# Performance work log

Hardware: AMD Instinct MI355X
Metric: run time of the kernel (lower is better)

Reference implementation:

```python
import jax, jax.numpy as jnp
import numpy as np
import math

T, B, C, H, W = 1, 64, 512, 8, 8
E, NH, MEM, FF = 512, 8, 32, 2048
HD = E // NH            # 64 per-head channels
TOT = HD * H * W        # 4096 = flattened per-head dim (channels x spatial)


def conv2d(x, w, b):
    # NCHW conv with 'same' padding, matching torch.nn.Conv2d(padding='same')
    y = jax.lax.conv_general_dilated(x, w, (1, 1), 'SAME',
                                     dimension_numbers=('NCHW', 'OIHW', 'NCHW'))
    return y + b[None, :, None, None]


def layernorm(x, w, b, eps=1e-5):
    # LayerNorm over (C,H,W) with elementwise affine, matching nn.LayerNorm((C,H,W))
    m = jnp.mean(x, axis=(1, 2, 3), keepdims=True)
    v = jnp.var(x, axis=(1, 2, 3), keepdims=True)
    return (x - m) * jax.lax.rsqrt(v + eps) * w[None] + b[None]


def setup_inputs() -> dict:
    key = jax.random.key(0)
    ks = jax.random.split(key, 16)
    s = 0.02
    inp = {
        'input': jax.random.normal(ks[0], (T, B, C, H, W), jnp.float32),
        'attn_mask': jax.random.randint(ks[1], (B * NH, T, MEM), 0, 2) == 1,
        'concat_k': jax.random.normal(ks[2], (B, MEM, NH, TOT), jnp.float32),
        'concat_v': jax.random.normal(ks[3], (B, MEM, NH, TOT), jnp.float32),
        'proj_w': jax.random.normal(ks[4], (3 * E, C, 3, 3), jnp.float32) * s,
        'proj_b': jnp.zeros((3 * E,), jnp.float32),
        'out_w': jax.random.normal(ks[5], (E, E, 3, 3), jnp.float32) * s,
        'out_b': jnp.zeros((E,), jnp.float32),
        'lin1_w': jax.random.normal(ks[6], (FF, E, 3, 3), jnp.float32) * s,
        'lin1_b': jnp.zeros((FF,), jnp.float32),
        'lin2_w': jax.random.normal(ks[7], (E, FF, 3, 3), jnp.float32) * s,
        'lin2_b': jnp.zeros((E,), jnp.float32),
        'n1_w': jnp.ones((E, H, W), jnp.float32),
        'n1_b': jnp.zeros((E, H, W), jnp.float32),
        'n2_w': jnp.ones((E, H, W), jnp.float32),
        'n2_b': jnp.zeros((E, H, W), jnp.float32),
        'pos_w': jax.random.normal(ks[8], (MEM, H * W * E), jnp.float32) * s,
        'pos_b': jax.random.uniform(ks[9], (MEM, NH), jnp.float32, -0.1, 0.1),
    }
    return inp


def reference(input, attn_mask, concat_k, concat_v, proj_w, proj_b, out_w, out_b,
              lin1_w, lin1_b, lin2_w, lin2_b, n1_w, n1_b, n2_w, n2_b, pos_w, pos_b):
    x = input.reshape(T * B, C, H, W)
    kqv = conv2d(x, proj_w, proj_b)                      # [B, 3E, H, W]
    k0, q0, v0 = kqv[:, :E], kqv[:, E:2 * E], kqv[:, 2 * E:]

    def split_heads(t):  # [T*B,E,H,W] -> [B*NH, T, TOT]
        return t.reshape(T, B * NH, HD, H, W).transpose(1, 0, 2, 3, 4).reshape(B * NH, T, TOT)

    k, q, v = split_heads(k0), split_heads(q0), split_heads(v0)
    q = q / math.sqrt(TOT)

    def mem_pre(c):  # [B,MEM,NH,TOT] -> [B*NH, MEM-1, TOT]
        return c[:, 1:].transpose(1, 0, 2, 3).reshape(MEM - 1, B * NH, TOT).transpose(1, 0, 2)

    k = jnp.concatenate([mem_pre(concat_k), k], axis=1)  # [B*NH, MEM, TOT]
    v = jnp.concatenate([mem_pre(concat_v), v], axis=1)

    # learned relative-position bias on keys and logits
    pw = jnp.broadcast_to(pos_w[:, None, :], (MEM, B, NH * TOT)).reshape(MEM, B * NH, TOT).transpose(1, 0, 2)
    pb = jnp.broadcast_to(pos_b[:, None, :], (MEM, B, NH)).reshape(MEM, B * NH).transpose(1, 0)
    k = k + pw

    mask = jnp.where(attn_mask, -jnp.inf, 0.0).astype(q.dtype)
    mask = mask.at[:, :, -1].set(5.0)                    # current step always attendable (+5 bias)
    logits = mask + jnp.einsum('bqd,bkd->bqk', q, k) + pb[:, None, :]
    w_attn = jax.nn.softmax(logits, axis=-1)             # [B*NH, T, MEM]
    attn = jnp.einsum('bqk,bkd->bqd', w_attn, v)         # [B*NH, T, TOT]
    attn = attn.transpose(1, 0, 2).reshape(B, E, H, W)

    out = conv2d(attn, out_w, out_b)
    ret_k = k.transpose(1, 0, 2).reshape(MEM, B, NH, TOT).transpose(1, 0, 2, 3)
    ret_v = v.transpose(1, 0, 2).reshape(MEM, B, NH, TOT).transpose(1, 0, 2, 3)

    # norm_first=False path
    out = out + x[:, :E]
    out = layernorm(out, n1_w, n1_b)
    ff = conv2d(jax.nn.relu(conv2d(out, lin1_w, lin1_b)), lin2_w, lin2_b)
    out = layernorm(out + ff, n2_w, n2_b)
    return (out[None], ret_k, ret_v)
```

## Files before the change

### kernel.cpp

```cpp
#include <hip/hip_runtime.h>
#include <hip/hip_bf16.h>
#include <stdint.h>

typedef __attribute__((ext_vector_type(8))) short bf16x8;
typedef __attribute__((ext_vector_type(4))) float f32x4;

static __device__ __forceinline__ unsigned short f2bf(float f) {
  union { float f; unsigned int u; } v; v.f = f;
  unsigned int u = v.u;
  return (unsigned short)((u + 0x7FFFu + ((u >> 16) & 1u)) >> 16);
}

static __device__ __forceinline__ void gld16(const void* g, void* l) {
  __builtin_amdgcn_global_load_lds(
      (const __attribute__((address_space(1))) unsigned int*)g,
      (__attribute__((address_space(3))) unsigned int*)l, 16, 0, 0);
}

__global__ __launch_bounds__(256) void k_zero(uint4* __restrict__ p, int n) {
  int i = blockIdx.x * 256 + threadIdx.x;
  if (i < n) p[i] = make_uint4(0u, 0u, 0u, 0u);
}

__global__ __launch_bounds__(256) void k_prep(
    const float* __restrict__ projw, const float* __restrict__ outw,
    const float* __restrict__ l1w, const float* __restrict__ l2w,
    const float* __restrict__ x,
    unsigned short* __restrict__ wbP, unsigned short* __restrict__ wbO,
    unsigned short* __restrict__ wbL1, unsigned short* __restrict__ wbL2,
    unsigned short* __restrict__ xp) {
  __shared__ float l[4608];
  int bid = blockIdx.x, t = threadIdx.x;
  if (bid < 6144) {
    const float* in; unsigned short* out; int o, C, c0;
    if (bid < 1536)      { in = projw; out = wbP;  o = bid;               C = 512;  c0 = 0; }
    else if (bid < 2048) { in = outw;  out = wbO;  o = bid - 1536;        C = 512;  c0 = 0; }
    else if (bid < 4096) { in = l1w;   out = wbL1; o = bid - 2048;        C = 512;  c0 = 0; }
    else                 { in = l2w;   out = wbL2; o = (bid - 4096) >> 2; C = 2048; c0 = ((bid - 4096) & 3) << 9; }
    const float* src = in + ((size_t)o * C + c0) * 9;
    for (int j = t; j < 4608; j += 256) l[j] = src[j];
    __syncthreads();
    unsigned short* dst = out + (size_t)o * 9 * C;
#pragma unroll
    for (int j = 0; j < 18; ++j) {
      int f = t * 18 + j;
      int tap = f >> 9, c = f & 511;
      dst[(size_t)tap * C + c0 + c] = f2bf(l[c * 9 + tap]);
    }
  } else {
    int idx = bid - 6144;
    int b = idx >> 3, c0 = (idx & 7) << 6;
    float (*lt)[65] = (float(*)[65])l;
    int cr = t >> 2, p0 = (t & 3) << 4;
    const float* src = x + ((size_t)b * 512 + c0 + cr) * 64 + p0;
#pragma unroll
    for (int j = 0; j < 4; ++j) {
      float4 v = *(const float4*)(src + j * 4);
      lt[cr][p0 + j * 4 + 0] = v.x; lt[cr][p0 + j * 4 + 1] = v.y;
      lt[cr][p0 + j * 4 + 2] = v.z; lt[cr][p0 + j * 4 + 3] = v.w;
    }
    __syncthreads();
    int pix = t >> 2, cc0 = (t & 3) << 4;
    size_t prow = (size_t)b * 100 + 11 + (pix >> 3) * 10 + (pix & 7);
    unsigned short pk[16];
#pragma unroll
    for (int j = 0; j < 16; ++j) pk[j] = f2bf(lt[cc0 + j][pix]);
    *(uint4*)(xp + prow * 512 + c0 + cc0) = *(const uint4*)pk;
    *(uint4*)(xp + prow * 512 + c0 + cc0 + 8) = *(const uint4*)(pk + 8);
  }
}

__global__ __launch_bounds__(256) void k_x2pad(const float* __restrict__ x,
                                               unsigned short* __restrict__ xp) {
  int b = blockIdx.x >> 3, c0 = (blockIdx.x & 7) << 6;
  int t = threadIdx.x;
  __shared__ float l[64][65];
  int cr = t >> 2, p0 = (t & 3) << 4;
  const float* src = x + ((size_t)b * 512 + c0 + cr) * 64 + p0;
#pragma unroll
  for (int j = 0; j < 4; ++j) {
    float4 v = *(const float4*)(src + j * 4);
    l[cr][p0 + j * 4 + 0] = v.x; l[cr][p0 + j * 4 + 1] = v.y;
    l[cr][p0 + j * 4 + 2] = v.z; l[cr][p0 + j * 4 + 3] = v.w;
  }
  __syncthreads();
  int pix = t >> 2, cc0 = (t & 3) << 4;
  size_t prow = (size_t)b * 100 + 11 + (pix >> 3) * 10 + (pix & 7);
  unsigned short pk[16];
#pragma unroll
  for (int j = 0; j < 16; ++j) pk[j] = f2bf(l[cc0 + j][pix]);
  *(uint4*)(xp + prow * 512 + c0 + cc0) = *(const uint4*)pk;
  *(uint4*)(xp + prow * 512 + c0 + cc0 + 8) = *(const uint4*)(pk + 8);
}

template <int EPI>
__global__ __launch_bounds__(256, 2) void k_gemm9(
    const unsigned short* __restrict__ Wt, int ldK,
    const unsigned short* __restrict__ Xp, int C, int tlog,
    int kiter, const float* __restrict__ bias,
    void* __restrict__ outv, int Cout, size_t zstride) {
  __shared__ unsigned short lds[2][2][8192];
  int t = threadIdx.x, lane = t & 63, wid = t >> 6;

  int gx = gridDim.x;
  int f = blockIdx.x + blockIdx.y * gx;
  int cpx = (gx * gridDim.y) >> 3;
  int fs = (f & 7) * cpx + (f >> 3);
  int bx = fs % gx, by = fs / gx;

  int O0 = bx << 7, M0 = by << 7;
  int kbase = blockIdx.z * kiter;
  int srow = lane >> 3, skg = (lane & 7) << 3;

  int wrow[4], pbv[4];
#pragma unroll
  for (int i = 0; i < 4; ++i) {
    int rl = wid * 8 + i * 32 + srow;
    wrow[i] = O0 + rl;
    int m = M0 + rl, b = m >> 6, pix = m & 63;
    pbv[i] = b * 100 + (pix >> 3) * 10 + (pix & 7);
  }

  f32x4 acc[4][4];
#pragma unroll
  for (int i = 0; i < 4; ++i)
#pragma unroll
    for (int j = 0; j < 4; ++j) acc[i][j] = (f32x4){0.f, 0.f, 0.f, 0.f};

  auto stage = [&](int buf, int kt) {
    int gk = kbase + kt;
    int tap = gk >> tlog;
    int c0 = (gk - (tap << tlog)) << 6;
    int toff = tap + 7 * ((tap * 11) >> 5);
#pragma unroll
    for (int i = 0; i < 4; ++i) {
      gld16(Wt + (size_t)wrow[i] * ldK + (gk << 6) + skg,
            &lds[buf][0][(wid * 8 + i * 32) * 64]);
      gld16(Xp + (size_t)(pbv[i] + toff) * C + c0 + skg,
            &lds[buf][1][(wid * 8 + i * 32) * 64]);
    }
  };

  int wr = wid >> 1, wc = wid & 1;
  int frow = lane & 15, fkb = (lane >> 4) << 3;

  auto compute = [&](int buf) {
    const unsigned short* Wl = &lds[buf][0][0];
    const unsigned short* Xl = &lds[buf][1][0];
#pragma unroll
    for (int kk = 0; kk < 2; ++kk) {
      bf16x8 af[4], bfv[4];
#pragma unroll
      for (int ff = 0; ff < 4; ++ff) {
        af[ff]  = *(const bf16x8*)(Wl + ((wr * 64 + ff * 16 + frow) << 6) + kk * 32 + fkb);
        bfv[ff] = *(const bf16x8*)(Xl + ((wc * 64 + ff * 16 + frow) << 6) + kk * 32 + fkb);
      }
#pragma unroll
      for (int fi = 0; fi < 4; ++fi)
#pragma unroll
        for (int fj = 0; fj < 4; ++fj)
          acc[fi][fj] = __builtin_amdgcn_mfma_f32_16x16x32_bf16(af[fi], bfv[fj], acc[fi][fj], 0, 0, 0);
    }
  };

  stage(0, 0);
  __syncthreads();
  for (int kt = 0; kt < kiter; ++kt) {
    int cur = kt & 1;
    if (kt + 1 < kiter) stage(cur ^ 1, kt + 1);
    compute(cur);
    __syncthreads();
  }

  int ob = O0 + wr * 64, mb = M0 + wc * 64;
  int r0 = (lane >> 4) << 2, cm = lane & 15;
  if (EPI == 4) {
    unsigned short* outp = (unsigned short*)outv;
#pragma unroll
    for (int fi = 0; fi < 4; ++fi) {
      int oo = ob + fi * 16 + r0;
      float4 bv = *(const float4*)(bias + oo);
#pragma unroll
      for (int fj = 0; fj < 4; ++fj) {
        int mm = mb + fj * 16 + cm;
        int bb = mm >> 6, pix = mm & 63;
        size_t prow = (size_t)bb * 100 + 11 + (pix >> 3) * 10 + (pix & 7);
        unsigned short pk[4];
        pk[0] = f2bf(fmaxf(acc[fi][fj][0] + bv.x, 0.f));
        pk[1] = f2bf(fmaxf(acc[fi][fj][1] + bv.y, 0.f));
        pk[2] = f2bf(fmaxf(acc[fi][fj][2] + bv.z, 0.f));
        pk[3] = f2bf(fmaxf(acc[fi][fj][3] + bv.w, 0.f));
        *(ushort4*)(outp + prow * Cout + oo) = *(const ushort4*)pk;
      }
    }
  } else {
    float* out = (float*)outv + (size_t)blockIdx.z * zstride;
#pragma unroll
    for (int fi = 0; fi < 4; ++fi) {
#pragma unroll
      for (int fj = 0; fj < 4; ++fj) {
        int mm = mb + fj * 16 + cm;
        int bb = mm >> 6, pix = mm & 63;
#pragma unroll
        for (int r = 0; r < 4; ++r) {
          int oo = ob + fi * 16 + r0 + r;
          float v = acc[fi][fj][r];
          if (EPI == 0) v += bias[oo];
          out[((size_t)bb * Cout + oo) * 64 + pix] = v;
        }
      }
    }
  }
}

__global__ __launch_bounds__(256) void k_sum2(const float* __restrict__ a,
                                              const float* __restrict__ b,
                                              const float* __restrict__ bias,
                                              float* __restrict__ o) {
  int i = (blockIdx.x * 256 + threadIdx.x) * 4;
  int ch = (i >> 6) % 1536;
  float4 va = *(const float4*)(a + i);
  float4 vb = *(const float4*)(b + i);
  float bs = bias[ch];
  *(float4*)(o + i) = make_float4(va.x + vb.x + bs, va.y + vb.y + bs,
                                  va.z + vb.z + bs, va.w + vb.w + bs);
}

__global__ __launch_bounds__(256) void k_attnK(
    const float* __restrict__ kqv, const float* __restrict__ ck,
    const float* __restrict__ pw, const float* __restrict__ pb,
    float* __restrict__ rk, float* __restrict__ logits) {
  int idx = blockIdx.x;
  int h = idx & 7, m = (idx >> 3) & 31, b = idx >> 8;
  int t = threadIdx.x, lane = t & 63, wid = t >> 6;
  int i0 = t << 4;
  int hd = i0 >> 6, pix = i0 & 63;

  const float* src = (m < 31)
      ? (ck + (((size_t)(b * 32 + m + 1) * 8 + h) << 12) + i0)
      : (kqv + ((size_t)(b * 1536 + h * 64 + hd) << 6) + pix);
  const float* qs = kqv + ((size_t)(b * 1536 + 512 + h * 64 + hd) << 6) + pix;
  const float* pws = pw + ((size_t)m << 15) + (h << 12) + i0;
  float* dst = rk + (((size_t)(b * 32 + m) * 8 + h) << 12) + i0;

  float part = 0.f;
#pragma unroll
  for (int j = 0; j < 4; ++j) {
    float4 a = *(const float4*)(src + j * 4);
    float4 p = *(const float4*)(pws + j * 4);
    float4 q = *(const float4*)(qs + j * 4);
    float4 kk;
    kk.x = a.x + p.x; kk.y = a.y + p.y; kk.z = a.z + p.z; kk.w = a.w + p.w;
    *(float4*)(dst + j * 4) = kk;
    part += 0.015625f * (q.x * kk.x + q.y * kk.y + q.z * kk.z + q.w * kk.w);
  }
#pragma unroll
  for (int s = 32; s; s >>= 1) part += __shfl_xor(part, s);
  __shared__ float red[4];
  if (lane == 0) red[wid] = part;
  __syncthreads();
  if (t == 0)
    logits[((b << 3) + h) * 32 + m] = red[0] + red[1] + red[2] + red[3] + pb[m * 8 + h];
}

__global__ __launch_bounds__(256) void k_attnV(
    const float* __restrict__ kqv, const int* __restrict__ mask,
    const float* __restrict__ cv, const float* __restrict__ logits,
    float* __restrict__ rv, float* __restrict__ attnb) {
  int bh = blockIdx.x, b = bh >> 3, h = bh & 7;
  int t = threadIdx.x;
  int d = (blockIdx.y << 10) + (t << 2);
  int hd = d >> 6, pix = d & 63;

  float lg[32];
#pragma unroll
  for (int j = 0; j < 8; ++j) {
    float4 v = *(const float4*)(logits + bh * 32 + j * 4);
    lg[j * 4 + 0] = v.x; lg[j * 4 + 1] = v.y; lg[j * 4 + 2] = v.z; lg[j * 4 + 3] = v.w;
  }
  float mx = -INFINITY;
#pragma unroll
  for (int m = 0; m < 32; ++m) {
    if (m == 31) lg[m] += 5.0f;
    else if (mask[bh * 32 + m] != 0) lg[m] = -INFINITY;
    mx = fmaxf(mx, lg[m]);
  }
  float sm = 0.f;
#pragma unroll
  for (int m = 0; m < 32; ++m) { lg[m] = __expf(lg[m] - mx); sm += lg[m]; }
  float rs = 1.f / sm;

  float4 acc = make_float4(0.f, 0.f, 0.f, 0.f);
  for (int m = 0; m < 32; ++m) {
    const float* src = (m < 31)
        ? (cv + (((size_t)(b * 32 + m + 1) * 8 + h) << 12) + d)
        : (kqv + ((size_t)(b * 1536 + 1024 + h * 64 + hd) << 6) + pix);
    float4 v = *(const float4*)src;
    *(float4*)(rv + (((size_t)(b * 32 + m) * 8 + h) << 12) + d) = v;
    float wm = lg[m] * rs;
    acc.x += wm * v.x; acc.y += wm * v.y; acc.z += wm * v.z; acc.w += wm * v.w;
  }
  *(float4*)(attnb + ((size_t)(b * 512 + h * 64 + hd) << 6) + pix) = acc;
}

__global__ __launch_bounds__(256) void k_lnstat(
    const float* __restrict__ p, const float* __restrict__ resid,
    const float* __restrict__ bias, float* __restrict__ xbuf,
    float2* __restrict__ stat) {
  int bb = blockIdx.x, seg = blockIdx.y, t = threadIdx.x;
  int lane = t & 63, wid = t >> 6;
  size_t base = (size_t)bb << 15;
  float s = 0.f, sq = 0.f;
#pragma unroll
  for (int j = 0; j < 4; ++j) {
    int i = (seg << 12) + t * 4 + j * 1024;
    float4 v0 = *(const float4*)(p + base + i);
    float4 v1 = *(const float4*)(p + 2097152 + base + i);
    float4 v2 = *(const float4*)(p + 4194304 + base + i);
    float4 v3 = *(const float4*)(p + 6291456 + base + i);
    float4 vr = *(const float4*)(resid + base + i);
    float bs = bias[i >> 6];
    float4 xx;
    xx.x = v0.x + v1.x + v2.x + v3.x + vr.x + bs;
    xx.y = v0.y + v1.y + v2.y + v3.y + vr.y + bs;
    xx.z = v0.z + v1.z + v2.z + v3.z + vr.z + bs;
    xx.w = v0.w + v1.w + v2.w + v3.w + vr.w + bs;
    *(float4*)(xbuf + base + i) = xx;
    s += xx.x + xx.y + xx.z + xx.w;
    sq += xx.x * xx.x + xx.y * xx.y + xx.z * xx.z + xx.w * xx.w;
  }
#pragma unroll
  for (int k = 32; k; k >>= 1) { s += __shfl_xor(s, k); sq += __shfl_xor(sq, k); }
  __shared__ float rsm[4], rqm[4];
  if (lane == 0) { rsm[wid] = s; rqm[wid] = sq; }
  __syncthreads();
  if (t == 0)
    stat[bb * 8 + seg] = make_float2(rsm[0] + rsm[1] + rsm[2] + rsm[3],
                                     rqm[0] + rqm[1] + rqm[2] + rqm[3]);
}

__global__ __launch_bounds__(256) void k_lnapply(
    const float* __restrict__ xbuf, const float2* __restrict__ stat,
    const float* __restrict__ w, const float* __restrict__ beta,
    float* __restrict__ out) {
  int bb = blockIdx.x, seg = blockIdx.y, t = threadIdx.x;
  size_t base = (size_t)bb << 15;
  float s = 0.f, sq = 0.f;
#pragma unroll
  for (int k = 0; k < 8; ++k) {
    float2 st = stat[bb * 8 + k];
    s += st.x; sq += st.y;
  }
  float mean = s * (1.f / 32768.f);
  float var = sq * (1.f / 32768.f) - mean * mean;
  float rinv = rsqrtf(var + 1e-5f);
#pragma unroll
  for (int j = 0; j < 4; ++j) {
    int i = (seg << 12) + t * 4 + j * 1024;
    float4 xx = *(const float4*)(xbuf + base + i);
    float4 vw = *(const float4*)(w + i);
    float4 vt = *(const float4*)(beta + i);
    float4 r;
    r.x = (xx.x - mean) * rinv * vw.x + vt.x;
    r.y = (xx.y - mean) * rinv * vw.y + vt.y;
    r.z = (xx.z - mean) * rinv * vw.z + vt.z;
    r.w = (xx.w - mean) * rinv * vw.w + vt.w;
    *(float4*)(out + base + i) = r;
  }
}

extern "C" void kernel_launch(void* const* d_in, const int* in_sizes, int n_in,
                              void* d_out, int out_size, void* d_ws, size_t ws_size,
                              hipStream_t stream) {
  const float* x     = (const float*)d_in[0];
  const int*   mask  = (const int*)d_in[1];
  const float* ck    = (const float*)d_in[2];
  const float* cv    = (const float*)d_in[3];
  const float* projw = (const float*)d_in[4];
  const float* projb = (const float*)d_in[5];
  const float* outw  = (const float*)d_in[6];
  const float* outb  = (const float*)d_in[7];
  const float* l1w   = (const float*)d_in[8];
  const float* l1b   = (const float*)d_in[9];
  const float* l2w   = (const float*)d_in[10];
  const float* l2b   = (const float*)d_in[11];
  const float* n1w   = (const float*)d_in[12];
  const float* n1b   = (const float*)d_in[13];
  const float* n2w   = (const float*)d_in[14];
  const float* n2b   = (const float*)d_in[15];
  const float* posw  = (const float*)d_in[16];
  const float* posb  = (const float*)d_in[17];

  char* ws = (char*)d_ws;
  unsigned short* wbP   = (unsigned short*)(ws);
  unsigned short* wbO   = (unsigned short*)(ws + 14155776);
  unsigned short* wbL1  = (unsigned short*)(ws + 18874368);
  unsigned short* wbL2  = (unsigned short*)(ws + 37748736);
  unsigned short* xpadI = (unsigned short*)(ws + 56623104);
  unsigned short* apad  = (unsigned short*)(ws + 63176704);
  unsigned short* l1pad = (unsigned short*)(ws + 69730304);
  unsigned short* ffpad = (unsigned short*)(ws + 76283904);
  float* kqvA   = (float*)(ws + 102498304);
  float* kqvB   = (float*)(ws + 127664128);
  float* kqv    = (float*)(ws + 152829952);
  float* logits = (float*)(ws + 177995776);
  float* res    = (float*)(ws + 178061312);
  float* ln1    = (float*)(ws + 211615744);
  float* attnb  = (float*)(ws + 220004352);
  float* xbuf1  = (float*)(ws + 228392960);
  float* xbuf2  = (float*)(ws + 236781568);
  float2* stat1 = (float2*)(ws + 245170176);
  float2* stat2 = (float2*)(ws + 245174272);

  float* out0 = (float*)d_out;
  float* rk = out0 + 2097152;
  float* rv = rk + 67108864;

  k_zero<<<11200, 256, 0, stream>>>((uint4*)(ws + 56623104), 2867200);

  k_prep<<<6656, 256, 0, stream>>>(projw, outw, l1w, l2w, x, wbP, wbO, wbL1, wbL2, xpadI);

  k_gemm9<3><<<dim3(12, 32, 2), 256, 0, stream>>>(wbP, 4608, xpadI, 512, 3, 36, nullptr, kqvA, 1536, 6291456);
  k_sum2<<<6144, 256, 0, stream>>>(kqvA, kqvB, projb, kqv);

  k_attnK<<<16384, 256, 0, stream>>>(kqv, ck, posw, posb, rk, logits);
  k_attnV<<<dim3(512, 4), 256, 0, stream>>>(kqv, mask, cv, logits, rv, attnb);
  k_x2pad<<<512, 256, 0, stream>>>(attnb, apad);

  k_gemm9<3><<<dim3(4, 32, 4), 256, 0, stream>>>(wbO, 4608, apad, 512, 3, 18, nullptr, res, 512, 2097152);
  k_lnstat<<<dim3(64, 8), 256, 0, stream>>>(res, x, outb, xbuf1, stat1);
  k_lnapply<<<dim3(64, 8), 256, 0, stream>>>(xbuf1, stat1, n1w, n1b, ln1);
  k_x2pad<<<512, 256, 0, stream>>>(ln1, l1pad);

  k_gemm9<4><<<dim3(16, 32, 1), 256, 0, stream>>>(wbL1, 4608, l1pad, 512, 3, 72, l1b, ffpad, 2048, 0);

  k_gemm9<3><<<dim3(4, 32, 4), 256, 0, stream>>>(wbL2, 18432, ffpad, 2048, 5, 72, nullptr, res, 512, 2097152);
  k_lnstat<<<dim3(64, 8), 256, 0, stream>>>(res, ln1, l2b, xbuf2, stat2);
  k_lnapply<<<dim3(64, 8), 256, 0, stream>>>(xbuf2, stat2, n2w, n2b, out0);
}
```

Baseline: 750.3 us.

## Overlap ret_k/ret_v copies with FFN GEMMs and fuse layernorm into padding

The bulk copies of ret_k and ret_v (memory shifted by one slot, plus the pos bias for k) move out of the attention kernels into extra blocks appended to the FFN conv GEMM launches, so that memory-bound copy work runs alongside compute-bound GEMM blocks. The GEMM grid is flattened to 1D, LDS drops from double to single buffering, and occupancy is raised to 3 blocks per CU. Only the pad border rows are zeroed now instead of the whole padded buffers, and the layernorm apply is fused with the bf16 pad conversion. Losing the double buffer exposes load latency in each k-step, and the copy blocks compete with the GEMMs for bandwidth and CU slots.

```diff
diff --git a/kernel.cpp b/kernel.cpp
--- a/kernel.cpp
+++ b/kernel.cpp
@@ -17,9 +17,23 @@
       (__attribute__((address_space(3))) unsigned int*)l, 16, 0, 0);
 }
 
-__global__ __launch_bounds__(256) void k_zero(uint4* __restrict__ p, int n) {
-  int i = blockIdx.x * 256 + threadIdx.x;
-  if (i < n) p[i] = make_uint4(0u, 0u, 0u, 0u);
+__global__ __launch_bounds__(256) void k_zero_border(
+    unsigned short* __restrict__ p0, unsigned short* __restrict__ p1,
+    unsigned short* __restrict__ p2, unsigned short* __restrict__ p3) {
+  int ridx = blockIdx.x % 36, b = blockIdx.x / 36, t = threadIdx.x;
+  int row;
+  if (ridx < 11) row = ridx;
+  else if (ridx < 25) { int p = ridx - 11; row = 19 + (p >> 1) * 10 + (p & 1); }
+  else row = 89 + (ridx - 25);
+  unsigned short* ptr; int C;
+  switch (blockIdx.y) {
+    case 0: ptr = p0; C = 512; break;
+    case 1: ptr = p1; C = 512; break;
+    case 2: ptr = p2; C = 512; break;
+    default: ptr = p3; C = 2048; break;
+  }
+  int n16 = C >> 3;
+  if (t < n16) *(uint4*)(ptr + ((size_t)b * 100 + row) * C + t * 8) = make_uint4(0u, 0u, 0u, 0u);
 }
 
 __global__ __launch_bounds__(256) void k_prep(
@@ -94,22 +108,58 @@
 }
 
 template <int EPI>
-__global__ __launch_bounds__(256, 2) void k_gemm9(
+__global__ __launch_bounds__(256, 3) void k_gemm9(
     const unsigned short* __restrict__ Wt, int ldK,
     const unsigned short* __restrict__ Xp, int C, int tlog,
     int kiter, const float* __restrict__ bias,
-    void* __restrict__ outv, int Cout, size_t zstride) {
-  __shared__ unsigned short lds[2][2][8192];
-  int t = threadIdx.x, lane = t & 63, wid = t >> 6;
-
-  int gx = gridDim.x;
-  int f = blockIdx.x + blockIdx.y * gx;
-  int cpx = (gx * gridDim.y) >> 3;
+    void* __restrict__ outv, int Cout, size_t zstride,
+    int gx, int nxy, int NS,
+    const float* __restrict__ s_src, const float* __restrict__ s_pw,
+    float* __restrict__ s_dst) {
+  __shared__ unsigned short lds[2][8192];
+  int t = threadIdx.x;
+  int nG = gridDim.x - NS;
+
+  if ((int)blockIdx.x >= nG) {
+    int id2 = blockIdx.x - nG;
+#pragma unroll
+    for (int uu = 0; uu < 2; ++uu) {
+      int u = id2 * 2 + uu;
+      int b = u / 248;
+      int rem = u - b * 248;
+      int m = rem >> 3, h = rem & 7;
+      const float* src = s_src + (((size_t)(b * 32 + m + 1) * 8 + h) << 12);
+      float* dst = s_dst + (((size_t)(b * 32 + m) * 8 + h) << 12);
+      if (s_pw) {
+        const float* pws = s_pw + ((size_t)m << 15) + (h << 12);
+#pragma unroll
+        for (int j = 0; j < 4; ++j) {
+          int i = t * 4 + j * 1024;
+          float4 a = *(const float4*)(src + i);
+          float4 p = *(const float4*)(pws + i);
+          *(float4*)(dst + i) = make_float4(a.x + p.x, a.y + p.y, a.z + p.z, a.w + p.w);
+        }
+      } else {
+#pragma unroll
+        for (int j = 0; j < 4; ++j) {
+          int i = t * 4 + j * 1024;
+          *(float4*)(dst + i) = *(const float4*)(src + i);
+        }
+      }
+    }
+    return;
+  }
+
+  int lane = t & 63, wid = t >> 6;
+  int id = blockIdx.x;
+  int bz = id / nxy;
+  int f = id - bz * nxy;
+  int cpx = nxy >> 3;
   int fs = (f & 7) * cpx + (f >> 3);
   int bx = fs % gx, by = fs / gx;
 
   int O0 = bx << 7, M0 = by << 7;
-  int kbase = blockIdx.z * kiter;
+  int kbase = bz * kiter;
   int srow = lane >> 3, skg = (lane & 7) << 3;
 
   int wrow[4], pbv[4];
@@ -127,7 +177,7 @@
 #pragma unroll
     for (int j = 0; j < 4; ++j) acc[i][j] = (f32x4){0.f, 0.f, 0.f, 0.f};
 
-  auto stage = [&](int buf, int kt) {
+  auto stage = [&](int kt) {
     int gk = kbase + kt;
     int tap = gk >> tlog;
     int c0 = (gk - (tap << tlog)) << 6;
@@ -135,18 +185,18 @@
 #pragma unroll
     for (int i = 0; i < 4; ++i) {
       gld16(Wt + (size_t)wrow[i] * ldK + (gk << 6) + skg,
-            &lds[buf][0][(wid * 8 + i * 32) * 64]);
+            &lds[0][(wid * 8 + i * 32) * 64]);
       gld16(Xp + (size_t)(pbv[i] + toff) * C + c0 + skg,
-            &lds[buf][1][(wid * 8 + i * 32) * 64]);
+            &lds[1][(wid * 8 + i * 32) * 64]);
     }
   };
 
   int wr = wid >> 1, wc = wid & 1;
   int frow = lane & 15, fkb = (lane >> 4) << 3;
 
-  auto compute = [&](int buf) {
-    const unsigned short* Wl = &lds[buf][0][0];
-    const unsigned short* Xl = &lds[buf][1][0];
+  auto compute = [&]() {
+    const unsigned short* Wl = &lds[0][0];
+    const unsigned short* Xl = &lds[1][0];
 #pragma unroll
     for (int kk = 0; kk < 2; ++kk) {
       bf16x8 af[4], bfv[4];
@@ -163,12 +213,10 @@
     }
   };
 
-  stage(0, 0);
-  __syncthreads();
   for (int kt = 0; kt < kiter; ++kt) {
-    int cur = kt & 1;
-    if (kt + 1 < kiter) stage(cur ^ 1, kt + 1);
-    compute(cur);
+    stage(kt);
+    __syncthreads();
+    compute();
     __syncthreads();
   }
 
@@ -194,7 +242,7 @@
       }
     }
   } else {
-    float* out = (float*)outv + (size_t)blockIdx.z * zstride;
+    float* out = (float*)outv + (size_t)bz * zstride;
 #pragma unroll
     for (int fi = 0; fi < 4; ++fi) {
 #pragma unroll
@@ -241,18 +289,21 @@
       : (kqv + ((size_t)(b * 1536 + h * 64 + hd) << 6) + pix);
   const float* qs = kqv + ((size_t)(b * 1536 + 512 + h * 64 + hd) << 6) + pix;
   const float* pws = pw + ((size_t)m << 15) + (h << 12) + i0;
-  float* dst = rk + (((size_t)(b * 32 + m) * 8 + h) << 12) + i0;
 
   float part = 0.f;
+  float4 kk[4];
 #pragma unroll
   for (int j = 0; j < 4; ++j) {
     float4 a = *(const float4*)(src + j * 4);
     float4 p = *(const float4*)(pws + j * 4);
     float4 q = *(const float4*)(qs + j * 4);
-    float4 kk;
-    kk.x = a.x + p.x; kk.y = a.y + p.y; kk.z = a.z + p.z; kk.w = a.w + p.w;
-    *(float4*)(dst + j * 4) = kk;
-    part += 0.015625f * (q.x * kk.x + q.y * kk.y + q.z * kk.z + q.w * kk.w);
+    kk[j].x = a.x + p.x; kk[j].y = a.y + p.y; kk[j].z = a.z + p.z; kk[j].w = a.w + p.w;
+    part += 0.015625f * (q.x * kk[j].x + q.y * kk[j].y + q.z * kk[j].z + q.w * kk[j].w);
+  }
+  if (m == 31) {
+    float* dst = rk + (((size_t)(b * 32 + 31) * 8 + h) << 12) + i0;
+#pragma unroll
+    for (int j = 0; j < 4; ++j) *(float4*)(dst + j * 4) = kk[j];
   }
 #pragma unroll
   for (int s = 32; s; s >>= 1) part += __shfl_xor(part, s);
@@ -291,13 +342,16 @@
   float rs = 1.f / sm;
 
   float4 acc = make_float4(0.f, 0.f, 0.f, 0.f);
-  for (int m = 0; m < 32; ++m) {
-    const float* src = (m < 31)
-        ? (cv + (((size_t)(b * 32 + m + 1) * 8 + h) << 12) + d)
-        : (kqv + ((size_t)(b * 1536 + 1024 + h * 64 + hd) << 6) + pix);
+  for (int m = 0; m < 31; ++m) {
+    const float* src = cv + (((size_t)(b * 32 + m + 1) * 8 + h) << 12) + d;
     float4 v = *(const float4*)src;
-    *(float4*)(rv + (((size_t)(b * 32 + m) * 8 + h) << 12) + d) = v;
     float wm = lg[m] * rs;
+    acc.x += wm * v.x; acc.y += wm * v.y; acc.z += wm * v.z; acc.w += wm * v.w;
+  }
+  {
+    float4 v = *(const float4*)(kqv + ((size_t)(b * 1536 + 1024 + h * 64 + hd) << 6) + pix);
+    *(float4*)(rv + (((size_t)(b * 32 + 31) * 8 + h) << 12) + d) = v;
+    float wm = lg[31] * rs;
     acc.x += wm * v.x; acc.y += wm * v.y; acc.z += wm * v.z; acc.w += wm * v.w;
   }
   *(float4*)(attnb + ((size_t)(b * 512 + h * 64 + hd) << 6) + pix) = acc;
@@ -367,6 +421,50 @@
     r.w = (xx.w - mean) * rinv * vw.w + vt.w;
     *(float4*)(out + base + i) = r;
   }
+}
+
+__global__ __launch_bounds__(256) void k_lnpad(
+    const float* __restrict__ xbuf, const float2* __restrict__ stat,
+    const float* __restrict__ w, const float* __restrict__ beta,
+    float* __restrict__ ln1, unsigned short* __restrict__ lp) {
+  int b = blockIdx.x >> 3, c0 = (blockIdx.x & 7) << 6;
+  int t = threadIdx.x;
+  float s = 0.f, sq = 0.f;
+#pragma unroll
+  for (int k = 0; k < 8; ++k) {
+    float2 st = stat[b * 8 + k];
+    s += st.x; sq += st.y;
+  }
+  float mean = s * (1.f / 32768.f);
+  float var = sq * (1.f / 32768.f) - mean * mean;
+  float rinv = rsqrtf(var + 1e-5f);
+
+  __shared__ float l[64][65];
+  int cr = t >> 2, p0 = (t & 3) << 4;
+  size_t off = ((size_t)b * 512 + c0 + cr) * 64 + p0;
+  size_t woff = ((size_t)(c0 + cr)) * 64 + p0;
+#pragma unroll
+  for (int j = 0; j < 4; ++j) {
+    float4 xx = *(const float4*)(xbuf + off + j * 4);
+    float4 vw = *(const float4*)(w + woff + j * 4);
+    float4 vt = *(const float4*)(beta + woff + j * 4);
+    float4 r;
+    r.x = (xx.x - mean) * rinv * vw.x + vt.x;
+    r.y = (xx.y - mean) * rinv * vw.y + vt.y;
+    r.z = (xx.z - mean) * rinv * vw.z + vt.z;
+    r.w = (xx.w - mean) * rinv * vw.w + vt.w;
+    *(float4*)(ln1 + off + j * 4) = r;
+    l[cr][p0 + j * 4 + 0] = r.x; l[cr][p0 + j * 4 + 1] = r.y;
+    l[cr][p0 + j * 4 + 2] = r.z; l[cr][p0 + j * 4 + 3] = r.w;
+  }
+  __syncthreads();
+  int pix = t >> 2, cc0 = (t & 3) << 4;
+  size_t prow = (size_t)b * 100 + 11 + (pix >> 3) * 10 + (pix & 7);
+  unsigned short pk[16];
+#pragma unroll
+  for (int j = 0; j < 16; ++j) pk[j] = f2bf(l[cc0 + j][pix]);
+  *(uint4*)(lp + prow * 512 + c0 + cc0) = *(const uint4*)pk;
+  *(uint4*)(lp + prow * 512 + c0 + cc0 + 8) = *(const uint4*)(pk + 8);
 }
 
 extern "C" void kernel_launch(void* const* d_in, const int* in_sizes, int n_in,
@@ -416,25 +514,28 @@
   float* rk = out0 + 2097152;
   float* rv = rk + 67108864;
 
-  k_zero<<<11200, 256, 0, stream>>>((uint4*)(ws + 56623104), 2867200);
+  k_zero_border<<<dim3(2304, 4), 256, 0, stream>>>(xpadI, apad, l1pad, ffpad);
 
   k_prep<<<6656, 256, 0, stream>>>(projw, outw, l1w, l2w, x, wbP, wbO, wbL1, wbL2, xpadI);
 
-  k_gemm9<3><<<dim3(12, 32, 2), 256, 0, stream>>>(wbP, 4608, xpadI, 512, 3, 36, nullptr, kqvA, 1536, 6291456);
+  k_gemm9<3><<<768, 256, 0, stream>>>(wbP, 4608, xpadI, 512, 3, 36, nullptr, kqvA, 1536, 6291456,
+                                      12, 384, 0, nullptr, nullptr, nullptr);
   k_sum2<<<6144, 256, 0, stream>>>(kqvA, kqvB, projb, kqv);
 
   k_attnK<<<16384, 256, 0, stream>>>(kqv, ck, posw, posb, rk, logits);
   k_attnV<<<dim3(512, 4), 256, 0, stream>>>(kqv, mask, cv, logits, rv, attnb);
   k_x2pad<<<512, 256, 0, stream>>>(attnb, apad);
 
-  k_gemm9<3><<<dim3(4, 32, 4), 256, 0, stream>>>(wbO, 4608, apad, 512, 3, 18, nullptr, res, 512, 2097152);
+  k_gemm9<3><<<512, 256, 0, stream>>>(wbO, 4608, apad, 512, 3, 18, nullptr, res, 512, 2097152,
+                                      4, 128, 0, nullptr, nullptr, nullptr);
   k_lnstat<<<dim3(64, 8), 256, 0, stream>>>(res, x, outb, xbuf1, stat1);
-  k_lnapply<<<dim3(64, 8), 256, 0, stream>>>(xbuf1, stat1, n1w, n1b, ln1);
-  k_x2pad<<<512, 256, 0, stream>>>(ln1, l1pad);
-
-  k_gemm9<4><<<dim3(16, 32, 1), 256, 0, stream>>>(wbL1, 4608, l1pad, 512, 3, 72, l1b, ffpad, 2048, 0);
-
-  k_gemm9<3><<<dim3(4, 32, 4), 256, 0, stream>>>(wbL2, 18432, ffpad, 2048, 5, 72, nullptr, res, 512, 2097152);
+  k_lnpad<<<512, 256, 0, stream>>>(xbuf1, stat1, n1w, n1b, ln1, l1pad);
+
+  k_gemm9<4><<<512 + 7936, 256, 0, stream>>>(wbL1, 4608, l1pad, 512, 3, 72, l1b, ffpad, 2048, 0,
+                                             16, 512, 7936, ck, posw, rk);
+
+  k_gemm9<3><<<512 + 7936, 256, 0, stream>>>(wbL2, 18432, ffpad, 2048, 5, 72, nullptr, res, 512, 2097152,
+                                             4, 128, 7936, cv, nullptr, rv);
   k_lnstat<<<dim3(64, 8), 256, 0, stream>>>(res, ln1, l2b, xbuf2, stat2);
   k_lnapply<<<dim3(64, 8), 256, 0, stream>>>(xbuf2, stat2, n2w, n2b, out0);
 }
```

After: 756.2 us. About the same (+0.8%).
